# Kernel tuning notes

Measured on AMD Instinct MI355X. Metric: run time of the kernel, lower is better.

## Reference

```python
import jax, jax.numpy as jnp
import numpy as np

B, L, C = 2, 2048, 1024
H, HD = 16, 64
MAX_SCALE_MUL = float(np.log(100.0))
SCALE = 1.0  # attn_l2_norm=True -> scale is 1


def setup_inputs() -> dict:
    key = jax.random.key(0)
    ks = jax.random.split(key, 6)
    x = jax.random.normal(ks[0], (B, L, C), dtype=jnp.float32)
    attn_bias = jax.random.normal(ks[1], (1, 1, L, L), dtype=jnp.float32)
    w_qkv = jax.random.normal(ks[2], (3 * C, C), dtype=jnp.float32) * (1.0 / np.sqrt(C))
    q_bias = jnp.zeros((C,), dtype=jnp.float32)
    v_bias = jnp.zeros((C,), dtype=jnp.float32)
    scale_mul = jnp.full((1, H, 1, 1), np.log(4.0), dtype=jnp.float32)  # scale_mul_1H11
    w_proj = jax.random.normal(ks[3], (C, C), dtype=jnp.float32) * (1.0 / np.sqrt(C))
    b_proj = jnp.zeros((C,), dtype=jnp.float32)
    return {"x": x, "attn_bias": attn_bias, "w_qkv": w_qkv, "q_bias": q_bias,
            "v_bias": v_bias, "scale_mul": scale_mul, "w_proj": w_proj, "b_proj": b_proj}


def reference(x, attn_bias, w_qkv, q_bias, v_bias, scale_mul, w_proj, b_proj):
    # qkv projection with concatenated bias (q_bias, zeros, v_bias)
    bias = jnp.concatenate([q_bias, jnp.zeros_like(q_bias), v_bias])  # [3C]
    qkv = jnp.einsum('blc,dc->bld', x, w_qkv) + bias                  # [B,L,3C]
    qkv = qkv.reshape(B, L, 3, H, HD).transpose(2, 0, 3, 1, 4)        # [3,B,H,L,HD]
    q, k, v = qkv[0], qkv[1], qkv[2]
    # attn_l2_norm path: L2-normalize q,k; q scaled by exp(clamped scale_mul)
    sm = jnp.exp(jnp.minimum(scale_mul, MAX_SCALE_MUL))               # [1,H,1,1]
    q = q / jnp.linalg.norm(q, axis=-1, keepdims=True) * sm
    k = k / jnp.linalg.norm(k, axis=-1, keepdims=True)
    # slow_attn: scaled scores + bias, softmax, weighted sum
    attn = jnp.einsum('bhld,bhmd->bhlm', q * SCALE, k) + attn_bias    # [B,H,L,L]
    p = jax.nn.softmax(attn, axis=-1)
    oup = jnp.einsum('bhlm,bhmd->bhld', p, v)                         # [B,H,L,HD]
    oup = oup.transpose(0, 2, 1, 3).reshape(B, L, C)
    return jnp.einsum('blc,dc->bld', oup, w_proj) + b_proj
```

## Files before the change

kernel.cpp:

```cpp
#include <hip/hip_runtime.h>
#include <cstdint>
#include <cstddef>
#include <math.h>

typedef __attribute__((ext_vector_type(8))) __bf16 bf16x8;
typedef __attribute__((ext_vector_type(4))) __bf16 bf16x4;
typedef __attribute__((ext_vector_type(4))) float f32x4;

#define AS1 __attribute__((address_space(1)))
#define AS3 __attribute__((address_space(3)))

#define LOG2E 1.4426950408889634f

__device__ __forceinline__ void gld16(void* lds_uniform, const void* gaddr) {
  __builtin_amdgcn_global_load_lds((const AS1 unsigned int*)gaddr,
                                   (AS3 unsigned int*)lds_uniform, 16, 0, 0);
}

__global__ __launch_bounds__(256)
void prep_kernel(const float* __restrict__ x, const float* __restrict__ wqkv,
                 const float* __restrict__ wproj, const float* __restrict__ bias,
                 __bf16* __restrict__ xb, __bf16* __restrict__ wqkvb,
                 __bf16* __restrict__ wprojb, __bf16* __restrict__ btr) {
  __shared__ __bf16 T[32][264];
  const int b = blockIdx.x;
  const int tid = threadIdx.x;
  if (b < 8192) {
    const float* src; __bf16* dst; int off;
    if (b < 4096)      { src = x;     dst = xb;     off = b; }
    else if (b < 7168) { src = wqkv;  dst = wqkvb;  off = b - 4096; }
    else               { src = wproj; dst = wprojb; off = b - 7168; }
    const int i = (off * 256 + tid) * 4;
    const float4 v = *(const float4*)(src + i);
    bf16x4 o;
    o[0] = (__bf16)v.x; o[1] = (__bf16)v.y; o[2] = (__bf16)v.z; o[3] = (__bf16)v.w;
    *(bf16x4*)(dst + i) = o;
    return;
  }
  const int bb = b - 8192;
  const int rb = bb >> 3, cg = bb & 7;
  const float* src = bias + (size_t)(rb * 32) * 2048 + cg * 256;
#pragma unroll
  for (int i = 0; i < 8; ++i) {
    const int u = i * 256 + tid;
    const int r = u >> 6, c4 = (u & 63) * 4;
    const float4 v = *(const float4*)(src + (size_t)r * 2048 + c4);
    T[r][c4 + 0] = (__bf16)(v.x * LOG2E);
    T[r][c4 + 1] = (__bf16)(v.y * LOG2E);
    T[r][c4 + 2] = (__bf16)(v.z * LOG2E);
    T[r][c4 + 3] = (__bf16)(v.w * LOG2E);
  }
  __syncthreads();
  const int ktl = tid >> 6;
  const int lane = tid & 63, g = lane >> 4, c = lane & 15;
  __bf16 outv[32];
#pragma unroll
  for (int v = 0; v < 32; ++v) {
    const int mi = v >> 4, ni = (v >> 2) & 3, j = v & 3;
    outv[v] = T[mi * 16 + g * 4 + j][ktl * 64 + ni * 16 + c];
  }
  __bf16* dst = btr + ((size_t)(rb * 32 + cg * 4 + ktl) * 64 + lane) * 32;
#pragma unroll
  for (int i = 0; i < 4; ++i)
    *(bf16x8*)(dst + i * 8) = *(bf16x8*)(outv + i * 8);
}

__global__ __launch_bounds__(256, 2)
void gemm_qkv_kernel(const __bf16* __restrict__ A, const __bf16* __restrict__ B,
                     const float* __restrict__ q_bias, const float* __restrict__ v_bias,
                     const float* __restrict__ scale_mul,
                     __bf16* __restrict__ qb, __bf16* __restrict__ ktp, __bf16* __restrict__ vb) {
  __shared__ __attribute__((aligned(16))) __bf16 As[128 * 32];
  __shared__ __attribute__((aligned(16))) __bf16 Bs[128 * 32];
  const int tid = threadIdx.x;
  const int w = tid >> 6, lane = tid & 63;
  const int m0 = blockIdx.y * 128, n0 = blockIdx.x * 128;
  const int wm = (w >> 1) * 64, wn = (w & 1) * 64;
  const int c = lane & 15, g = lane >> 4;
  f32x4 acc[4][4];
#pragma unroll
  for (int i = 0; i < 4; ++i)
#pragma unroll
    for (int j = 0; j < 4; ++j) acc[i][j] = (f32x4)(0.0f);

  const int r_row = lane >> 2;
  const int r_col = (lane & 3) * 16;
  const char* Abase = (const char*)A + (size_t)m0 * 2048;
  const char* Bbase = (const char*)B + (size_t)n0 * 2048;

  for (int kt = 0; kt < 1024; kt += 32) {
#pragma unroll
    for (int s = 0; s < 2; ++s) {
      const int R = w * 2 + s;
      const int row = R * 16 + r_row;
      gld16((char*)As + R * 1024, Abase + (size_t)row * 2048 + kt * 2 + r_col);
      gld16((char*)Bs + R * 1024, Bbase + (size_t)row * 2048 + kt * 2 + r_col);
    }
    __syncthreads();
    bf16x8 af[4], bfr[4];
#pragma unroll
    for (int i = 0; i < 4; ++i) {
      af[i]  = *(const bf16x8*)((const char*)As + (wm + i * 16 + c) * 64 + g * 16);
      bfr[i] = *(const bf16x8*)((const char*)Bs + (wn + i * 16 + c) * 64 + g * 16);
    }
#pragma unroll
    for (int ni = 0; ni < 4; ++ni)
#pragma unroll
      for (int mi = 0; mi < 4; ++mi)
        acc[ni][mi] = __builtin_amdgcn_mfma_f32_16x16x32_bf16(bfr[ni], af[mi], acc[ni][mi], 0, 0, 0);
    __syncthreads();
  }

  const int nbase = n0 + wn;
  const int which = nbase >> 10;
  const int h = (nbase >> 6) & 15;
  float smh = 1.0f;
  if (which == 0) smh = __expf(fminf(scale_mul[h], 4.605170185988091f)) * LOG2E;
  float4 cb[4];
#pragma unroll
  for (int ni = 0; ni < 4; ++ni) {
    if (which == 0)      cb[ni] = *(const float4*)(q_bias + nbase + ni * 16 + 4 * g);
    else if (which == 2) cb[ni] = *(const float4*)(v_bias + nbase - 2048 + ni * 16 + 4 * g);
    else                 cb[ni] = make_float4(0.f, 0.f, 0.f, 0.f);
  }
  const int mrow0 = m0 + wm;
  const int b2 = mrow0 >> 11;
  const int lpos0 = mrow0 & 2047;
  __bf16* kt_tile = ktp + (size_t)(b2 * 16 + h) * 131072 + (size_t)(lpos0 >> 6) * 4096;
  __bf16* dst_qv = ((which == 0) ? qb : vb) + ((size_t)((b2 * 16 + h) * 2048 + lpos0)) * 64;

#pragma unroll
  for (int mi = 0; mi < 4; ++mi) {
    float v[4][4];
    float ss = 0.0f;
#pragma unroll
    for (int ni = 0; ni < 4; ++ni) {
      v[ni][0] = acc[ni][mi][0] + cb[ni].x;
      v[ni][1] = acc[ni][mi][1] + cb[ni].y;
      v[ni][2] = acc[ni][mi][2] + cb[ni].z;
      v[ni][3] = acc[ni][mi][3] + cb[ni].w;
#pragma unroll
      for (int j = 0; j < 4; ++j) ss += v[ni][j] * v[ni][j];
    }
    ss += __shfl_xor(ss, 16, 64);
    ss += __shfl_xor(ss, 32, 64);
    const float sc = (which == 2) ? 1.0f : (rsqrtf(ss) * smh);
    const int key = mi * 16 + c;
    if (which == 1) {
#pragma unroll
      for (int ni = 0; ni < 4; ++ni) {
        bf16x4 pk;
        pk[0] = (__bf16)(v[ni][0] * sc); pk[1] = (__bf16)(v[ni][1] * sc);
        pk[2] = (__bf16)(v[ni][2] * sc); pk[3] = (__bf16)(v[ni][3] * sc);
        *(bf16x4*)(kt_tile + (ni >> 1) * 2048 + key * 32 + (ni & 1) * 16 + 4 * g) = pk;
      }
    } else {
      __bf16* drow = dst_qv + (size_t)key * 64;
#pragma unroll
      for (int ni = 0; ni < 4; ++ni) {
        bf16x4 pk;
        pk[0] = (__bf16)(v[ni][0] * sc); pk[1] = (__bf16)(v[ni][1] * sc);
        pk[2] = (__bf16)(v[ni][2] * sc); pk[3] = (__bf16)(v[ni][3] * sc);
        *(bf16x4*)(drow + ni * 16 + 4 * g) = pk;
      }
    }
  }
}

__global__ __launch_bounds__(256)
void vtrans_kernel(const __bf16* __restrict__ vb, __bf16* __restrict__ vtp) {
  __shared__ __attribute__((aligned(16))) __bf16 Vs[4][64 * 64];
  const int w = threadIdx.x >> 6, lane = threadIdx.x & 63;
  const int idx = blockIdx.x * 4 + w;
  const int bh = idx >> 5, tile = idx & 31;
  const __bf16* src = vb + ((size_t)bh * 2048 + tile * 64) * 64;
#pragma unroll
  for (int s = 0; s < 8; ++s)
    gld16((char*)&Vs[w][0] + s * 1024, (const char*)src + s * 1024 + lane * 16);
  __syncthreads();
  __bf16* outb = vtp + (size_t)idx * 4096;
#pragma unroll
  for (int r = 0; r < 8; ++r) {
    const int o = r * 512 + lane * 8;
    const int hd = (o >> 5) & 63;
    const int sl0 = ((o >> 11) << 5) | (o & 31);
    bf16x8 pk;
#pragma unroll
    for (int i = 0; i < 8; ++i) {
      const int slot = sl0 + i;
      const int key = (slot & 3) * 16 + (slot >> 2);
      pk[i] = Vs[w][key * 64 + hd];
    }
    *(bf16x8*)(outb + o) = pk;
  }
}

#define STAGE(t, b) {                                                          \
  const char* _ks = kp + (size_t)(t) * 8192 + w * 2048 + lane * 16;            \
  const char* _vs = vp + (size_t)(t) * 8192 + w * 2048 + lane * 16;            \
  gld16(&Kb[b][w * 2048],        _ks);                                         \
  gld16(&Kb[b][w * 2048 + 1024], _ks + 1024);                                  \
  gld16(&Vb[b][w * 2048],        _vs);                                         \
  gld16(&Vb[b][w * 2048 + 1024], _vs + 1024);                                  \
}

#define COMPUTE(t, b) {                                                        \
  bf16x8 kf[4][2];                                                             \
  _Pragma("unroll")                                                            \
  for (int ni = 0; ni < 4; ++ni)                                               \
    _Pragma("unroll")                                                          \
    for (int ks = 0; ks < 2; ++ks)                                             \
      kf[ni][ks] = *(const bf16x8*)(&Kb[b][0] + ks * 4096 + (ni * 16 + c) * 64 + g * 16); \
  f32x4 sacc[2][4];                                                            \
  _Pragma("unroll")                                                            \
  for (int mi = 0; mi < 2; ++mi)                                               \
    _Pragma("unroll")                                                          \
    for (int ni = 0; ni < 4; ++ni) {                                           \
      f32x4 s_ = __builtin_amdgcn_mfma_f32_16x16x32_bf16(qf[mi][0], kf[ni][0], (f32x4)(0.0f), 0, 0, 0); \
      sacc[mi][ni] = __builtin_amdgcn_mfma_f32_16x16x32_bf16(qf[mi][1], kf[ni][1], s_, 0, 0, 0); \
    }                                                                          \
  const char* _bb = bp + ((size_t)(t) * 64 + lane) * 64;                       \
  bf16x8 bA[4];                                                                \
  _Pragma("unroll")                                                            \
  for (int i = 0; i < 4; ++i) bA[i] = *(const bf16x8*)(_bb + i * 16);          \
  _Pragma("unroll")                                                            \
  for (int mi = 0; mi < 2; ++mi)                                               \
    _Pragma("unroll")                                                          \
    for (int j = 0; j < 4; ++j) {                                              \
      const float p0 = __builtin_amdgcn_exp2f(sacc[mi][0][j] + (float)bA[(mi * 16 + 0 + j) >> 3][(mi * 16 + 0 + j) & 7]);  \
      const float p1 = __builtin_amdgcn_exp2f(sacc[mi][1][j] + (float)bA[(mi * 16 + 4 + j) >> 3][(mi * 16 + 4 + j) & 7]);  \
      const float p2 = __builtin_amdgcn_exp2f(sacc[mi][2][j] + (float)bA[(mi * 16 + 8 + j) >> 3][(mi * 16 + 8 + j) & 7]);  \
      const float p3 = __builtin_amdgcn_exp2f(sacc[mi][3][j] + (float)bA[(mi * 16 + 12 + j) >> 3][(mi * 16 + 12 + j) & 7]);\
      lsum[mi][j] += (p0 + p1) + (p2 + p3);                                    \
      bf16x4 pk;                                                               \
      pk[0] = (__bf16)p0; pk[1] = (__bf16)p1; pk[2] = (__bf16)p2; pk[3] = (__bf16)p3; \
      *(bf16x4*)&Ps[w][c >> 3][mi * 16 + g * 4 + j][(c & 7) * 4] = pk;         \
    }                                                                          \
  bf16x8 pf[2][2];                                                             \
  _Pragma("unroll")                                                            \
  for (int mi = 0; mi < 2; ++mi)                                               \
    _Pragma("unroll")                                                          \
    for (int ks = 0; ks < 2; ++ks)                                             \
      pf[mi][ks] = *(const bf16x8*)&Ps[w][ks][mi * 16 + c][g * 8];             \
  _Pragma("unroll")                                                            \
  for (int ni = 0; ni < 4; ++ni) {                                             \
    const bf16x8 v0 = *(const bf16x8*)(&Vb[b][0] + 0 * 4096 + ni * 1024 + c * 64 + g * 16); \
    const bf16x8 v1 = *(const bf16x8*)(&Vb[b][0] + 1 * 4096 + ni * 1024 + c * 64 + g * 16); \
    _Pragma("unroll")                                                          \
    for (int mi = 0; mi < 2; ++mi) {                                           \
      oacc[mi][ni] = __builtin_amdgcn_mfma_f32_16x16x32_bf16(pf[mi][0], v0, oacc[mi][ni], 0, 0, 0); \
      oacc[mi][ni] = __builtin_amdgcn_mfma_f32_16x16x32_bf16(pf[mi][1], v1, oacc[mi][ni], 0, 0, 0); \
    }                                                                          \
  }                                                                            \
}

__global__ __launch_bounds__(256, 3)
void attn_kernel(const __bf16* __restrict__ qb, const __bf16* __restrict__ ktp,
                 const __bf16* __restrict__ vtp, const __bf16* __restrict__ btr,
                 __bf16* __restrict__ oupb) {
  __shared__ __attribute__((aligned(16))) char Kb[2][8192];
  __shared__ __attribute__((aligned(16))) char Vb[2][8192];
  __shared__ __attribute__((aligned(16))) __bf16 Ps[4][2][32][40];
  const int tid = threadIdx.x, w = tid >> 6, lane = tid & 63;
  const int c = lane & 15, g = lane >> 4;
  const int idx = blockIdx.x;
  const int bh = idx & 31, rb = idx >> 5;
  const __bf16* qh = qb + (size_t)bh * (2048 * 64);
  const char* kp = (const char*)ktp + (size_t)bh * (32 * 8192);
  const char* vp = (const char*)vtp + (size_t)bh * (32 * 8192);
  const int rb32 = rb * 4 + w;
  const char* bp = (const char*)btr + (size_t)rb32 * 131072;
  const int q0 = rb * 128 + w * 32;
  const int b2 = bh >> 4, h = bh & 15;

  bf16x8 qf[2][2];
#pragma unroll
  for (int mi = 0; mi < 2; ++mi)
#pragma unroll
    for (int ks = 0; ks < 2; ++ks)
      qf[mi][ks] = *(const bf16x8*)(qh + (size_t)(q0 + mi * 16 + c) * 64 + ks * 32 + g * 8);

  f32x4 oacc[2][4];
  float lsum[2][4];
#pragma unroll
  for (int mi = 0; mi < 2; ++mi)
#pragma unroll
    for (int ni = 0; ni < 4; ++ni) oacc[mi][ni] = (f32x4)(0.0f);
#pragma unroll
  for (int mi = 0; mi < 2; ++mi)
#pragma unroll
    for (int j = 0; j < 4; ++j) lsum[mi][j] = 0.0f;

  STAGE(0, 0);
  __syncthreads();
#pragma unroll 1
  for (int tt = 0; tt < 32; tt += 2) {
    if (tt + 1 < 32) STAGE(tt + 1, 1);
    COMPUTE(tt, 0);
    __syncthreads();
    if (tt + 2 < 32) STAGE(tt + 2, 0);
    COMPUTE(tt + 1, 1);
    __syncthreads();
  }

#pragma unroll
  for (int mi = 0; mi < 2; ++mi)
#pragma unroll
    for (int j = 0; j < 4; ++j) {
      float l = lsum[mi][j];
      l += __shfl_xor(l, 1, 64);
      l += __shfl_xor(l, 2, 64);
      l += __shfl_xor(l, 4, 64);
      l += __shfl_xor(l, 8, 64);
      const float inv = 1.0f / l;
      const int qrow = q0 + mi * 16 + g * 4 + j;
      __bf16* orow = oupb + ((size_t)(b2 * 2048 + qrow) * 16 + h) * 64;
#pragma unroll
      for (int ni = 0; ni < 4; ++ni)
        orow[ni * 16 + c] = (__bf16)(oacc[mi][ni][j] * inv);
    }
}

__global__ __launch_bounds__(256, 2)
void gemm_proj_kernel(const __bf16* __restrict__ A, const __bf16* __restrict__ B,
                      const float* __restrict__ b_proj, float* __restrict__ out) {
  __shared__ __attribute__((aligned(16))) __bf16 As[64 * 32];
  __shared__ __attribute__((aligned(16))) __bf16 Bs[128 * 32];
  const int tid = threadIdx.x;
  const int w = tid >> 6, lane = tid & 63;
  const int c = lane & 15, g = lane >> 4;
  const int m0 = blockIdx.y * 64, n0 = blockIdx.x * 128;
  const int wm = (w >> 1) * 32, wn = (w & 1) * 64;
  f32x4 acc[2][4];
#pragma unroll
  for (int i = 0; i < 2; ++i)
#pragma unroll
    for (int j = 0; j < 4; ++j) acc[i][j] = (f32x4)(0.0f);

  const int r_row = lane >> 2;
  const int r_col = (lane & 3) * 16;
  const char* Abase = (const char*)A + (size_t)m0 * 2048;
  const char* Bbase = (const char*)B + (size_t)n0 * 2048;

  for (int kt = 0; kt < 1024; kt += 32) {
    {
      const int row = w * 16 + r_row;
      gld16((char*)As + w * 1024, Abase + (size_t)row * 2048 + kt * 2 + r_col);
    }
#pragma unroll
    for (int s = 0; s < 2; ++s) {
      const int R = w * 2 + s;
      const int row = R * 16 + r_row;
      gld16((char*)Bs + R * 1024, Bbase + (size_t)row * 2048 + kt * 2 + r_col);
    }
    __syncthreads();
    bf16x8 af[2], bfr[4];
#pragma unroll
    for (int i = 0; i < 2; ++i)
      af[i] = *(const bf16x8*)((const char*)As + (wm + i * 16 + c) * 64 + g * 16);
#pragma unroll
    for (int i = 0; i < 4; ++i)
      bfr[i] = *(const bf16x8*)((const char*)Bs + (wn + i * 16 + c) * 64 + g * 16);
#pragma unroll
    for (int mi = 0; mi < 2; ++mi)
#pragma unroll
      for (int ni = 0; ni < 4; ++ni)
        acc[mi][ni] = __builtin_amdgcn_mfma_f32_16x16x32_bf16(af[mi], bfr[ni], acc[mi][ni], 0, 0, 0);
    __syncthreads();
  }

  float cbias[4];
#pragma unroll
  for (int ni = 0; ni < 4; ++ni) cbias[ni] = b_proj[n0 + wn + ni * 16 + c];
#pragma unroll
  for (int mi = 0; mi < 2; ++mi)
#pragma unroll
    for (int j = 0; j < 4; ++j) {
      const int m = m0 + wm + mi * 16 + g * 4 + j;
      float* orow = out + (size_t)m * 1024 + n0 + wn;
#pragma unroll
      for (int ni = 0; ni < 4; ++ni)
        orow[ni * 16 + c] = acc[mi][ni][j] + cbias[ni];
    }
}

extern "C" void kernel_launch(void* const* d_in, const int* in_sizes, int n_in,
                              void* d_out, int out_size, void* d_ws, size_t ws_size,
                              hipStream_t stream) {
  const float* x         = (const float*)d_in[0];
  const float* attn_bias = (const float*)d_in[1];
  const float* w_qkv     = (const float*)d_in[2];
  const float* q_bias    = (const float*)d_in[3];
  const float* v_bias    = (const float*)d_in[4];
  const float* scale_mul = (const float*)d_in[5];
  const float* w_proj    = (const float*)d_in[6];
  const float* b_proj    = (const float*)d_in[7];
  float* out = (float*)d_out;

  __bf16* xb     = (__bf16*)d_ws;
  __bf16* wqkvb  = xb + 4194304;
  __bf16* wprojb = wqkvb + 3145728;
  __bf16* qb     = wprojb + 1048576;
  __bf16* ktp    = qb + 4194304;
  __bf16* vtp    = ktp + 4194304;
  __bf16* btr    = vtp + 4194304;
  __bf16* vb     = btr + 4194304;
  __bf16* oupb   = xb;

  prep_kernel<<<8704, 256, 0, stream>>>(x, w_qkv, w_proj, attn_bias, xb, wqkvb, wprojb, btr);
  gemm_qkv_kernel<<<dim3(24, 32), 256, 0, stream>>>(xb, wqkvb, q_bias, v_bias, scale_mul,
                                                    qb, ktp, vb);
  vtrans_kernel<<<256, 256, 0, stream>>>(vb, vtp);
  attn_kernel<<<512, 256, 0, stream>>>(qb, ktp, vtp, btr, oupb);
  gemm_proj_kernel<<<dim3(8, 64), 256, 0, stream>>>(oupb, wprojb, b_proj, out);
}
```

Baseline: 221.3 us.

## Split attention work across 8 waves with 16 rows each and swizzled LDS

```diff
diff --git a/kernel.cpp b/kernel.cpp
--- a/kernel.cpp
+++ b/kernel.cpp
@@ -196,100 +196,89 @@
 }
 
 #define STAGE(t, b) {                                                          \
-  const char* _ks = kp + (size_t)(t) * 8192 + w * 2048 + lane * 16;            \
-  const char* _vs = vp + (size_t)(t) * 8192 + w * 2048 + lane * 16;            \
-  gld16(&Kb[b][w * 2048],        _ks);                                         \
-  gld16(&Kb[b][w * 2048 + 1024], _ks + 1024);                                  \
-  gld16(&Vb[b][w * 2048],        _vs);                                         \
-  gld16(&Vb[b][w * 2048 + 1024], _vs + 1024);                                  \
+  const char* _ks = kp + (size_t)(t) * 8192 + w * 1024 + sl16;                 \
+  const char* _vs = vp + (size_t)(t) * 8192 + w * 1024 + sl16;                 \
+  gld16(&Kb[b][w * 1024], _ks);                                                \
+  gld16(&Vb[b][w * 1024], _vs);                                                \
 }
 
 #define COMPUTE(t, b) {                                                        \
+  const char* _bb = bp + ((size_t)(t) * 64 + lane) * 64 + MI * 32;             \
+  bf16x8 bA[2];                                                                \
+  bA[0] = *(const bf16x8*)_bb;                                                 \
+  bA[1] = *(const bf16x8*)(_bb + 16);                                          \
   bf16x8 kf[4][2];                                                             \
   _Pragma("unroll")                                                            \
   for (int ni = 0; ni < 4; ++ni)                                               \
     _Pragma("unroll")                                                          \
     for (int ks = 0; ks < 2; ++ks)                                             \
-      kf[ni][ks] = *(const bf16x8*)(&Kb[b][0] + ks * 4096 + (ni * 16 + c) * 64 + g * 16); \
-  f32x4 sacc[2][4];                                                            \
-  _Pragma("unroll")                                                            \
-  for (int mi = 0; mi < 2; ++mi)                                               \
-    _Pragma("unroll")                                                          \
-    for (int ni = 0; ni < 4; ++ni) {                                           \
-      f32x4 s_ = __builtin_amdgcn_mfma_f32_16x16x32_bf16(qf[mi][0], kf[ni][0], (f32x4)(0.0f), 0, 0, 0); \
-      sacc[mi][ni] = __builtin_amdgcn_mfma_f32_16x16x32_bf16(qf[mi][1], kf[ni][1], s_, 0, 0, 0); \
-    }                                                                          \
-  const char* _bb = bp + ((size_t)(t) * 64 + lane) * 64;                       \
-  bf16x8 bA[4];                                                                \
-  _Pragma("unroll")                                                            \
-  for (int i = 0; i < 4; ++i) bA[i] = *(const bf16x8*)(_bb + i * 16);          \
-  _Pragma("unroll")                                                            \
-  for (int mi = 0; mi < 2; ++mi)                                               \
-    _Pragma("unroll")                                                          \
-    for (int j = 0; j < 4; ++j) {                                              \
-      const float p0 = __builtin_amdgcn_exp2f(sacc[mi][0][j] + (float)bA[(mi * 16 + 0 + j) >> 3][(mi * 16 + 0 + j) & 7]);  \
-      const float p1 = __builtin_amdgcn_exp2f(sacc[mi][1][j] + (float)bA[(mi * 16 + 4 + j) >> 3][(mi * 16 + 4 + j) & 7]);  \
-      const float p2 = __builtin_amdgcn_exp2f(sacc[mi][2][j] + (float)bA[(mi * 16 + 8 + j) >> 3][(mi * 16 + 8 + j) & 7]);  \
-      const float p3 = __builtin_amdgcn_exp2f(sacc[mi][3][j] + (float)bA[(mi * 16 + 12 + j) >> 3][(mi * 16 + 12 + j) & 7]);\
-      lsum[mi][j] += (p0 + p1) + (p2 + p3);                                    \
-      bf16x4 pk;                                                               \
-      pk[0] = (__bf16)p0; pk[1] = (__bf16)p1; pk[2] = (__bf16)p2; pk[3] = (__bf16)p3; \
-      *(bf16x4*)&Ps[w][c >> 3][mi * 16 + g * 4 + j][(c & 7) * 4] = pk;         \
-    }                                                                          \
-  bf16x8 pf[2][2];                                                             \
-  _Pragma("unroll")                                                            \
-  for (int mi = 0; mi < 2; ++mi)                                               \
-    _Pragma("unroll")                                                          \
-    for (int ks = 0; ks < 2; ++ks)                                             \
-      pf[mi][ks] = *(const bf16x8*)&Ps[w][ks][mi * 16 + c][g * 8];             \
+      kf[ni][ks] = *(const bf16x8*)(&Kb[b][0] + ks * 4096 + (ni * 16 + c) * 64 + gsw16); \
+  f32x4 sacc[4];                                                               \
+  __builtin_amdgcn_s_setprio(1);                                               \
   _Pragma("unroll")                                                            \
   for (int ni = 0; ni < 4; ++ni) {                                             \
-    const bf16x8 v0 = *(const bf16x8*)(&Vb[b][0] + 0 * 4096 + ni * 1024 + c * 64 + g * 16); \
-    const bf16x8 v1 = *(const bf16x8*)(&Vb[b][0] + 1 * 4096 + ni * 1024 + c * 64 + g * 16); \
-    _Pragma("unroll")                                                          \
-    for (int mi = 0; mi < 2; ++mi) {                                           \
-      oacc[mi][ni] = __builtin_amdgcn_mfma_f32_16x16x32_bf16(pf[mi][0], v0, oacc[mi][ni], 0, 0, 0); \
-      oacc[mi][ni] = __builtin_amdgcn_mfma_f32_16x16x32_bf16(pf[mi][1], v1, oacc[mi][ni], 0, 0, 0); \
-    }                                                                          \
+    f32x4 s_ = __builtin_amdgcn_mfma_f32_16x16x32_bf16(qf[0], kf[ni][0], (f32x4)(0.0f), 0, 0, 0); \
+    sacc[ni] = __builtin_amdgcn_mfma_f32_16x16x32_bf16(qf[1], kf[ni][1], s_, 0, 0, 0); \
   }                                                                            \
-}
-
-__global__ __launch_bounds__(256, 3)
+  __builtin_amdgcn_s_setprio(0);                                               \
+  _Pragma("unroll")                                                            \
+  for (int j = 0; j < 4; ++j) {                                                \
+    const float p0 = __builtin_amdgcn_exp2f(sacc[0][j] + (float)bA[(0 + j) >> 3][(0 + j) & 7]);   \
+    const float p1 = __builtin_amdgcn_exp2f(sacc[1][j] + (float)bA[(4 + j) >> 3][(4 + j) & 7]);   \
+    const float p2 = __builtin_amdgcn_exp2f(sacc[2][j] + (float)bA[(8 + j) >> 3][(8 + j) & 7]);   \
+    const float p3 = __builtin_amdgcn_exp2f(sacc[3][j] + (float)bA[(12 + j) >> 3][(12 + j) & 7]); \
+    lsum[j] += (p0 + p1) + (p2 + p3);                                          \
+    bf16x4 pk;                                                                 \
+    pk[0] = (__bf16)p0; pk[1] = (__bf16)p1; pk[2] = (__bf16)p2; pk[3] = (__bf16)p3; \
+    *(bf16x4*)&Ps[w][c >> 3][g * 4 + j][(c & 7) * 4] = pk;                     \
+  }                                                                            \
+  bf16x8 pf[2];                                                                \
+  _Pragma("unroll")                                                            \
+  for (int ks = 0; ks < 2; ++ks)                                               \
+    pf[ks] = *(const bf16x8*)&Ps[w][ks][c][g * 8];                             \
+  __builtin_amdgcn_s_setprio(1);                                               \
+  _Pragma("unroll")                                                            \
+  for (int ni = 0; ni < 4; ++ni) {                                             \
+    const bf16x8 v0 = *(const bf16x8*)(&Vb[b][0] + ni * 1024 + c * 64 + gsw16);        \
+    const bf16x8 v1 = *(const bf16x8*)(&Vb[b][0] + 4096 + ni * 1024 + c * 64 + gsw16); \
+    oacc[ni] = __builtin_amdgcn_mfma_f32_16x16x32_bf16(pf[0], v0, oacc[ni], 0, 0, 0);  \
+    oacc[ni] = __builtin_amdgcn_mfma_f32_16x16x32_bf16(pf[1], v1, oacc[ni], 0, 0, 0);  \
+  }                                                                            \
+  __builtin_amdgcn_s_setprio(0);                                               \
+}
+
+__global__ __launch_bounds__(512, 4)
 void attn_kernel(const __bf16* __restrict__ qb, const __bf16* __restrict__ ktp,
                  const __bf16* __restrict__ vtp, const __bf16* __restrict__ btr,
                  __bf16* __restrict__ oupb) {
   __shared__ __attribute__((aligned(16))) char Kb[2][8192];
   __shared__ __attribute__((aligned(16))) char Vb[2][8192];
-  __shared__ __attribute__((aligned(16))) __bf16 Ps[4][2][32][40];
+  __shared__ __attribute__((aligned(16))) __bf16 Ps[8][2][16][40];
   const int tid = threadIdx.x, w = tid >> 6, lane = tid & 63;
   const int c = lane & 15, g = lane >> 4;
+  const int MI = w & 1;
+  const int sl16 = (lane ^ ((lane >> 3) & 3)) * 16;
+  const int gsw16 = (g ^ ((c >> 1) & 3)) * 16;
   const int idx = blockIdx.x;
   const int bh = idx & 31, rb = idx >> 5;
   const __bf16* qh = qb + (size_t)bh * (2048 * 64);
   const char* kp = (const char*)ktp + (size_t)bh * (32 * 8192);
   const char* vp = (const char*)vtp + (size_t)bh * (32 * 8192);
-  const int rb32 = rb * 4 + w;
-  const char* bp = (const char*)btr + (size_t)rb32 * 131072;
-  const int q0 = rb * 128 + w * 32;
+  const char* bp = (const char*)btr + (size_t)(rb * 4 + (w >> 1)) * 131072;
+  const int q0 = rb * 128 + w * 16;
   const int b2 = bh >> 4, h = bh & 15;
 
-  bf16x8 qf[2][2];
-#pragma unroll
-  for (int mi = 0; mi < 2; ++mi)
-#pragma unroll
-    for (int ks = 0; ks < 2; ++ks)
-      qf[mi][ks] = *(const bf16x8*)(qh + (size_t)(q0 + mi * 16 + c) * 64 + ks * 32 + g * 8);
-
-  f32x4 oacc[2][4];
-  float lsum[2][4];
-#pragma unroll
-  for (int mi = 0; mi < 2; ++mi)
-#pragma unroll
-    for (int ni = 0; ni < 4; ++ni) oacc[mi][ni] = (f32x4)(0.0f);
-#pragma unroll
-  for (int mi = 0; mi < 2; ++mi)
-#pragma unroll
-    for (int j = 0; j < 4; ++j) lsum[mi][j] = 0.0f;
+  bf16x8 qf[2];
+#pragma unroll
+  for (int ks = 0; ks < 2; ++ks)
+    qf[ks] = *(const bf16x8*)(qh + (size_t)(q0 + c) * 64 + ks * 32 + g * 8);
+
+  f32x4 oacc[4];
+  float lsum[4];
+#pragma unroll
+  for (int ni = 0; ni < 4; ++ni) oacc[ni] = (f32x4)(0.0f);
+#pragma unroll
+  for (int j = 0; j < 4; ++j) lsum[j] = 0.0f;
 
   STAGE(0, 0);
   __syncthreads();
@@ -304,21 +293,19 @@
   }
 
 #pragma unroll
-  for (int mi = 0; mi < 2; ++mi)
-#pragma unroll
-    for (int j = 0; j < 4; ++j) {
-      float l = lsum[mi][j];
-      l += __shfl_xor(l, 1, 64);
-      l += __shfl_xor(l, 2, 64);
-      l += __shfl_xor(l, 4, 64);
-      l += __shfl_xor(l, 8, 64);
-      const float inv = 1.0f / l;
-      const int qrow = q0 + mi * 16 + g * 4 + j;
-      __bf16* orow = oupb + ((size_t)(b2 * 2048 + qrow) * 16 + h) * 64;
-#pragma unroll
-      for (int ni = 0; ni < 4; ++ni)
-        orow[ni * 16 + c] = (__bf16)(oacc[mi][ni][j] * inv);
-    }
+  for (int j = 0; j < 4; ++j) {
+    float l = lsum[j];
+    l += __shfl_xor(l, 1, 64);
+    l += __shfl_xor(l, 2, 64);
+    l += __shfl_xor(l, 4, 64);
+    l += __shfl_xor(l, 8, 64);
+    const float inv = 1.0f / l;
+    const int qrow = q0 + g * 4 + j;
+    __bf16* orow = oupb + ((size_t)(b2 * 2048 + qrow) * 16 + h) * 64;
+#pragma unroll
+    for (int ni = 0; ni < 4; ++ni)
+      orow[ni * 16 + c] = (__bf16)(oacc[ni][j] * inv);
+  }
 }
 
 __global__ __launch_bounds__(256, 2)
@@ -411,6 +398,6 @@
   gemm_qkv_kernel<<<dim3(24, 32), 256, 0, stream>>>(xb, wqkvb, q_bias, v_bias, scale_mul,
                                                     qb, ktp, vb);
   vtrans_kernel<<<256, 256, 0, stream>>>(vb, vtp);
-  attn_kernel<<<512, 256, 0, stream>>>(qb, ktp, vtp, btr, oupb);
+  attn_kernel<<<512, 512, 0, stream>>>(qb, ktp, vtp, btr, oupb);
   gemm_proj_kernel<<<dim3(8, 64), 256, 0, stream>>>(oupb, wprojb, b_proj, out);
 }
```

Result: no change. 218.1 us (-1.4%).
